# Kernel tuning notes

Measured on AMD Instinct MI355X. Metric: run time of the kernel, lower is better.

Reference implementation:

```python
import jax, jax.numpy as jnp
import numpy as np
from jax import lax

T = 16384          # num_tokens
H = 512            # hidden_size
HC = 4             # hc_mult
NGRAM = 4          # max_ngram_size -> conv dilation
N_EMBED = 256      # n_embed_per_ngram
N_HEADPN = 4       # n_head_per_ngram
NUM_HEADS = (NGRAM - 1) * N_HEADPN          # 12 embedding heads
HEAD_DIM = N_EMBED // N_HEADPN              # 64
E = (NGRAM - 1) * N_EMBED                   # 768 = engram_hidden_size
VOCAB = 50000
K = 4              # conv kernel_size
EPS = 1e-5         # layernorm_eps
GATE_EPS = 1e-6


def setup_inputs() -> dict:
    key = jax.random.key(0)
    ks = jax.random.split(key, 8)
    hash_ids = jax.random.randint(ks[0], (T, NUM_HEADS), 0, VOCAB, dtype=jnp.int32)
    offsets = jnp.asarray(np.concatenate([[0], np.cumsum([VOCAB] * (NUM_HEADS - 1))]).astype(np.int32))
    embedding_weight = jax.random.normal(ks[1], (NUM_HEADS * VOCAB, HEAD_DIM), jnp.float32) * 0.02
    key_projs_w = jax.random.normal(ks[2], (HC, E, H), jnp.float32) * 0.02
    q_norm_w = jnp.ones((HC, H), jnp.float32)
    k_norm_w = jnp.ones((HC, H), jnp.float32)
    v_proj_w = jax.random.normal(ks[3], (E, H), jnp.float32) * 0.02
    conv_w = jax.random.normal(ks[4], (HC * H, K), jnp.float32) * 0.1
    conv_norm_w = jnp.ones((HC, H), jnp.float32)
    hidden_states = jax.random.normal(ks[5], (T, HC, H), jnp.float32)
    return {
        'hash_ids': hash_ids, 'offsets': offsets, 'embedding_weight': embedding_weight,
        'key_projs_w': key_projs_w, 'q_norm_w': q_norm_w, 'k_norm_w': k_norm_w,
        'v_proj_w': v_proj_w, 'conv_w': conv_w, 'conv_norm_w': conv_norm_w,
        'hidden_states': hidden_states,
    }


def _group_rms_norm(x, w, eps=EPS):
    # x: [G, T, H], w: [G, H]; RMS over last dim, per-group affine scale
    inv = lax.rsqrt(jnp.mean(x * x, axis=-1, keepdims=True) + eps)
    return x * inv * w[:, None, :]


def reference(hash_ids, offsets, embedding_weight, key_projs_w, q_norm_w, k_norm_w,
              v_proj_w, conv_w, conv_norm_w, hidden_states):
    num_tokens, hc_mult, hidden = hidden_states.shape
    # --- MultiHeadEmbedding: hash-indexed gather into a concatenated table ---
    emb = embedding_weight[hash_ids + offsets[None, :]]          # [T, NUM_HEADS, HEAD_DIM]
    emb = emb.reshape(num_tokens, E)                              # [T, E]
    # --- key projection per hc group (bmm) ---
    keys = jnp.einsum('te,geh->gth', emb, key_projs_w)            # [HC, T, H]
    key_n = _group_rms_norm(keys, k_norm_w)
    query_n = _group_rms_norm(hidden_states.transpose(1, 0, 2), q_norm_w)  # [HC, T, H]
    # --- scaled dot-product gate ---
    scale = 1.0 / jnp.sqrt(jnp.asarray(hidden, hidden_states.dtype))
    gate = jax.nn.sigmoid(jnp.sum(key_n * query_n, axis=-1) * scale)       # [HC, T]
    gate = gate.T[:, :, None]                                     # [T, HC, 1]
    # --- value projection + gating ---
    value = gate * (emb @ v_proj_w)[:, None, :]                   # [T, HC, H]
    # --- ShortConv: GroupRMSNorm + depthwise dilated causal conv1d + SiLU ---
    x_n = _group_rms_norm(value.transpose(1, 0, 2), conv_norm_w)  # [HC, T, H]
    x_bct = x_n.transpose(0, 2, 1).reshape(1, hc_mult * hidden, num_tokens)  # [1, C, T]
    pad = NGRAM * (K - 1)
    y = lax.conv_general_dilated(
        x_bct, conv_w[:, None, :],                                # kernel [C, 1, K]
        window_strides=(1,), padding=[(pad, 0)], rhs_dilation=(NGRAM,),
        feature_group_count=hc_mult * hidden,
        dimension_numbers=('NCH', 'OIH', 'NCH'))
    y = jax.nn.silu(y)[0]                                         # [C, T]
    y = y.reshape(hc_mult, hidden, num_tokens).transpose(2, 0, 1) # [T, HC, H]
    return value + y


if __name__ == '__main__':
    out = reference(**setup_inputs())
    print(out.shape, out.dtype)
```

## Files before the change

kernel.cpp:

```cpp
#include <hip/hip_runtime.h>
#include <hip/hip_bf16.h>
#include <math.h>

#define T_TOK  16384
#define H_DIM  512
#define NHEADS 12
#define E_DIM  768
#define EPS_N  1e-5f
#define QK_SCALE 0.04419417382415922f

typedef unsigned short u16;
typedef __bf16 bf16;
typedef bf16   bf16x8 __attribute__((ext_vector_type(8)));
typedef float  f32x4  __attribute__((ext_vector_type(4)));
typedef u16    u16x8  __attribute__((ext_vector_type(8)));

__device__ __forceinline__ u16 f2bf(float f) {
  unsigned u = __builtin_bit_cast(unsigned, f);
  unsigned r = u + 0x7fffu + ((u >> 16) & 1u);
  return (u16)(r >> 16);
}
__device__ __forceinline__ float bf2f(u16 h) {
  unsigned u = ((unsigned)h) << 16;
  return __builtin_bit_cast(float, u);
}

__global__ __launch_bounds__(256) void gather_emb(
    const int* __restrict__ hash_ids, const int* __restrict__ offsets,
    const float* __restrict__ emb_w, u16* __restrict__ emb) {
  int idx = blockIdx.x * 256 + threadIdx.x;
  int pair = idx >> 3;
  int sub = idx & 7;
  int t = pair / 12;
  int head = pair - t * 12;
  int row = hash_ids[pair] + offsets[head];
  const float* src = emb_w + (size_t)row * 64 + sub * 8;
  float4 a = *(const float4*)src;
  float4 b = *(const float4*)(src + 4);
  u16x8 o;
  o[0] = f2bf(a.x); o[1] = f2bf(a.y); o[2] = f2bf(a.z); o[3] = f2bf(a.w);
  o[4] = f2bf(b.x); o[5] = f2bf(b.y); o[6] = f2bf(b.z); o[7] = f2bf(b.w);
  *(u16x8*)(emb + (size_t)t * E_DIM + head * 64 + sub * 8) = o;
}

__global__ __launch_bounds__(256) void build_wcat(
    const float* __restrict__ kp, const float* __restrict__ vp,
    u16* __restrict__ wt) {
  __shared__ float tile[32][33];
  int m = blockIdx.z;
  const float* src = (m < 4) ? (kp + (size_t)m * E_DIM * H_DIM) : vp;
  int h0 = blockIdx.x * 32, e0 = blockIdx.y * 32;
  int tx = threadIdx.x, ty = threadIdx.y;
  #pragma unroll
  for (int j = 0; j < 32; j += 8)
    tile[ty + j][tx] = src[(size_t)(e0 + ty + j) * H_DIM + h0 + tx];
  __syncthreads();
  #pragma unroll
  for (int j = 0; j < 32; j += 8) {
    int h = h0 + ty + j, e = e0 + tx;
    wt[(size_t)(m * H_DIM + h) * E_DIM + e] = f2bf(tile[tx][ty + j]);
  }
}

__global__ __launch_bounds__(256) void build_wc(
    const float* __restrict__ conv_w, const float* __restrict__ cnw,
    float* __restrict__ wc) {
  int cf = blockIdx.x * 256 + threadIdx.x;
  float c = cnw[cf];
  #pragma unroll
  for (int k = 0; k < 4; ++k) wc[k * 2048 + cf] = conv_w[cf * 4 + k] * c;
}

__global__ __launch_bounds__(256, 2) void gemm_bf16(
    const u16* __restrict__ A, const u16* __restrict__ BT,
    const float* __restrict__ hidden, const float* __restrict__ qw,
    const float* __restrict__ kw,
    u16* __restrict__ V, float* __restrict__ kssP, float* __restrict__ qkP,
    float* __restrict__ qssP, float* __restrict__ msvP) {
  __shared__ u16 As[128][64];
  __shared__ u16 Bs[128][64];
  __shared__ float part[2][128][3];
  const int K = E_DIM;
  int tid = threadIdx.x;
  int lane = tid & 63, wid = tid >> 6;
  int bx = blockIdx.x, by = blockIdx.y;
  int wm = (wid >> 1) * 64, wn = (wid & 1) * 64;
  int widN = wid & 1;

  const u16* aptr = A + (size_t)(by * 128 + (tid >> 3)) * K + (tid & 7) * 8;
  const u16* bptr = BT + (size_t)(bx * 128 + (tid >> 3)) * K + (tid & 7) * 8;
  int lds_off = tid * 16;

  f32x4 acc[4][4] = {};

  for (int k0 = 0; k0 < K; k0 += 64) {
    #pragma unroll
    for (int r = 0; r < 4; ++r) {
      __builtin_amdgcn_global_load_lds(
        (const __attribute__((address_space(1))) void*)(aptr + (size_t)(r * 32) * K + k0),
        (__attribute__((address_space(3))) void*)((char*)&As[0][0] + r * 4096 + lds_off),
        16, 0, 0);
      __builtin_amdgcn_global_load_lds(
        (const __attribute__((address_space(1))) void*)(bptr + (size_t)(r * 32) * K + k0),
        (__attribute__((address_space(3))) void*)((char*)&Bs[0][0] + r * 4096 + lds_off),
        16, 0, 0);
    }
    __syncthreads();
    int lr = lane & 15, lk8 = (lane >> 4) * 8;
    #pragma unroll
    for (int kk = 0; kk < 2; ++kk) {
      bf16x8 af[4], bfv[4];
      #pragma unroll
      for (int m = 0; m < 4; ++m)
        af[m] = *reinterpret_cast<const bf16x8*>(&As[wm + m * 16 + lr][kk * 32 + lk8]);
      #pragma unroll
      for (int n = 0; n < 4; ++n)
        bfv[n] = *reinterpret_cast<const bf16x8*>(&Bs[wn + n * 16 + lr][kk * 32 + lk8]);
      #pragma unroll
      for (int m = 0; m < 4; ++m)
        #pragma unroll
        for (int n = 0; n < 4; ++n)
          acc[m][n] = __builtin_amdgcn_mfma_f32_16x16x32_bf16(af[m], bfv[n], acc[m][n], 0, 0, 0);
    }
    __syncthreads();
  }

  int lr16 = lane & 15, rgrp = lane >> 4;

  if (bx < 16) {
    int g = bx >> 2, q = bx & 3;
    int colbase = g * 512 + q * 128 + wn + lr16;
    float qwv[4], kwv[4];
    #pragma unroll
    for (int n = 0; n < 4; ++n) {
      qwv[n] = qw[colbase + n * 16];
      kwv[n] = kw[colbase + n * 16];
    }
    #pragma unroll
    for (int m = 0; m < 4; ++m) {
      #pragma unroll
      for (int j = 0; j < 4; ++j) {
        int r = wm + m * 16 + rgrp * 4 + j;
        size_t t = (size_t)(by * 128 + r);
        float sk2 = 0.f, sqk = 0.f, sq2 = 0.f;
        #pragma unroll
        for (int n = 0; n < 4; ++n) {
          float kv = acc[m][n][j];
          float qv = hidden[t * 2048 + colbase + n * 16];
          sk2 += kv * kv;
          sqk += (qv * qwv[n]) * (kv * kwv[n]);
          sq2 += qv * qv;
        }
        #pragma unroll
        for (int off = 1; off < 16; off <<= 1) {
          sk2 += __shfl_xor(sk2, off, 64);
          sqk += __shfl_xor(sqk, off, 64);
          sq2 += __shfl_xor(sq2, off, 64);
        }
        if (lr16 == 0) {
          part[widN][r][0] = sk2;
          part[widN][r][1] = sqk;
          part[widN][r][2] = sq2;
        }
      }
    }
    __syncthreads();
    if (tid < 128) {
      int t = by * 128 + tid;
      int o = (t * 4 + g) * 4 + q;
      kssP[o] = part[0][tid][0] + part[1][tid][0];
      qkP[o]  = part[0][tid][1] + part[1][tid][1];
      qssP[o] = part[0][tid][2] + part[1][tid][2];
    }
  } else {
    int q2 = bx - 16;
    #pragma unroll
    for (int m = 0; m < 4; ++m) {
      #pragma unroll
      for (int j = 0; j < 4; ++j) {
        int r = wm + m * 16 + rgrp * 4 + j;
        size_t t = (size_t)(by * 128 + r);
        float sv2 = 0.f;
        #pragma unroll
        for (int n = 0; n < 4; ++n) {
          float v = acc[m][n][j];
          sv2 += v * v;
          V[t * 512 + q2 * 128 + wn + n * 16 + lr16] = f2bf(v);
        }
        #pragma unroll
        for (int off = 1; off < 16; off <<= 1) sv2 += __shfl_xor(sv2, off, 64);
        if (lr16 == 0) part[widN][r][0] = sv2;
      }
    }
    __syncthreads();
    if (tid < 128) {
      int t = by * 128 + tid;
      msvP[t * 4 + q2] = part[0][tid][0] + part[1][tid][0];
    }
  }
}

__global__ __launch_bounds__(256) void gate_finish(
    const float* __restrict__ kssP, const float* __restrict__ qkP,
    const float* __restrict__ qssP, const float* __restrict__ msvP,
    float* __restrict__ gateA, float* __restrict__ aA) {
  int i = blockIdx.x * 256 + threadIdx.x;
  int t = i >> 2;
  float4 k4 = *(const float4*)&kssP[i * 4];
  float4 d4 = *(const float4*)&qkP[i * 4];
  float4 q4 = *(const float4*)&qssP[i * 4];
  float4 m4 = *(const float4*)&msvP[t * 4];
  float kss = k4.x + k4.y + k4.z + k4.w;
  float qk  = d4.x + d4.y + d4.z + d4.w;
  float qss = q4.x + q4.y + q4.z + q4.w;
  float msv = (m4.x + m4.y + m4.z + m4.w) * (1.0f / 512.0f);
  float qinv = rsqrtf(qss * (1.0f / 512.0f) + EPS_N);
  float kinv = rsqrtf(kss * (1.0f / 512.0f) + EPS_N);
  float gate = 1.0f / (1.0f + __expf(-qk * qinv * kinv * QK_SCALE));
  gateA[i] = gate;
  aA[i] = gate * rsqrtf(gate * gate * msv + EPS_N);
}

__global__ __launch_bounds__(256) void out_kernel(
    const u16* __restrict__ V,
    const float* __restrict__ gateA, const float* __restrict__ aA,
    const float* __restrict__ wc,
    float* __restrict__ out) {
  int idx = blockIdx.x * 256 + threadIdx.x;
  int t = idx >> 8;
  int c8 = (idx & 255) * 8;
  int g = c8 >> 9;
  int h = c8 & 511;

  float acc[8] = {0.f, 0.f, 0.f, 0.f, 0.f, 0.f, 0.f, 0.f};
  float vr_t[8];
  #pragma unroll
  for (int k = 0; k < 4; ++k) {
    int tk = t - 12 + 4 * k;
    if (tk < 0) continue;
    float s = aA[tk * 4 + g];
    u16x8 vv = *(const u16x8*)&V[(size_t)tk * 512 + h];
    float4 w0 = *(const float4*)(wc + k * 2048 + c8);
    float4 w1 = *(const float4*)(wc + k * 2048 + c8 + 4);
    float w8[8] = {w0.x, w0.y, w0.z, w0.w, w1.x, w1.y, w1.z, w1.w};
    #pragma unroll
    for (int j = 0; j < 8; ++j) {
      float v = bf2f(vv[j]);
      acc[j] += w8[j] * s * v;
      if (k == 3) vr_t[j] = v;
    }
  }
  float gate = gateA[t * 4 + g];
  float r[8];
  #pragma unroll
  for (int j = 0; j < 8; ++j) {
    float y = acc[j];
    r[j] = gate * vr_t[j] + y / (1.0f + __expf(-y));
  }
  float* op = out + (size_t)t * 2048 + c8;
  *(float4*)op       = make_float4(r[0], r[1], r[2], r[3]);
  *(float4*)(op + 4) = make_float4(r[4], r[5], r[6], r[7]);
}

extern "C" void kernel_launch(void* const* d_in, const int* in_sizes, int n_in,
                              void* d_out, int out_size, void* d_ws, size_t ws_size,
                              hipStream_t stream) {
  const int*   hash_ids = (const int*)d_in[0];
  const int*   offsets  = (const int*)d_in[1];
  const float* emb_w    = (const float*)d_in[2];
  const float* kp       = (const float*)d_in[3];
  const float* qw       = (const float*)d_in[4];
  const float* kw       = (const float*)d_in[5];
  const float* vp       = (const float*)d_in[6];
  const float* conv_w   = (const float*)d_in[7];
  const float* cw       = (const float*)d_in[8];
  const float* hidden   = (const float*)d_in[9];
  float* out = (float*)d_out;
  char*  ws  = (char*)d_ws;

  u16*   V     = (u16*)ws;
  u16*   emb   = (u16*)(ws + 16777216);
  u16*   wt    = (u16*)(ws + 41943040);
  float* kssP  = (float*)(ws + 45875200);
  float* qkP   = (float*)(ws + 46923776);
  float* qssP  = (float*)(ws + 47972352);
  float* msvP  = (float*)(ws + 49020928);
  float* gateA = (float*)(ws + 49283072);
  float* aA    = (float*)(ws + 49545216);
  float* wc    = (float*)(ws + 49807360);

  gather_emb<<<(T_TOK * 12 * 8) / 256, 256, 0, stream>>>(hash_ids, offsets, emb_w, emb);
  build_wcat<<<dim3(16, 24, 5), dim3(32, 8), 0, stream>>>(kp, vp, wt);
  build_wc<<<8, 256, 0, stream>>>(conv_w, cw, wc);
  gemm_bf16<<<dim3(20, 128), 256, 0, stream>>>(emb, wt, hidden, qw, kw,
                                               V, kssP, qkP, qssP, msvP);
  gate_finish<<<(T_TOK * 4) / 256, 256, 0, stream>>>(kssP, qkP, qssP, msvP, gateA, aA);
  out_kernel<<<T_TOK * 256 / 256, 256, 0, stream>>>(V, gateA, aA, wc, out);
}
```

Before: 196.6 us.

## Precompute weighted bf16 query in fragment layout and per-token query norms

Adds a prep_q kernel that reads hidden_states once, computes the per-group query sum of squares, and writes q*q_norm_w as bf16 in a layout matching the GEMM accumulator fragments. The GEMM epilogue then reads packed bf16 query vectors, prefetched before the K loop, instead of strided fp32 hidden loads, and no longer computes the query norm. This aims to cut scattered fp32 reads in the epilogue and overlap the query fetch with the main loop. The cost is an extra kernel launch, an extra full pass over hidden plus a 64 MB intermediate write and read, higher register pressure from holding qf across the GEMM, and bf16 rounding of the query.

```diff
diff --git a/kernel.cpp b/kernel.cpp
--- a/kernel.cpp
+++ b/kernel.cpp
@@ -13,6 +13,7 @@
 typedef __bf16 bf16;
 typedef bf16   bf16x8 __attribute__((ext_vector_type(8)));
 typedef float  f32x4  __attribute__((ext_vector_type(4)));
+typedef u16    u16x4  __attribute__((ext_vector_type(4)));
 typedef u16    u16x8  __attribute__((ext_vector_type(8)));
 
 __device__ __forceinline__ u16 f2bf(float f) {
@@ -23,6 +24,11 @@
 __device__ __forceinline__ float bf2f(u16 h) {
   unsigned u = ((unsigned)h) << 16;
   return __builtin_bit_cast(float, u);
+}
+__device__ __forceinline__ float wave_sum(float v) {
+  #pragma unroll
+  for (int off = 32; off; off >>= 1) v += __shfl_xor(v, off, 64);
+  return v;
 }
 
 __global__ __launch_bounds__(256) void gather_emb(
@@ -71,25 +77,67 @@
   for (int k = 0; k < 4; ++k) wc[k * 2048 + cf] = conv_w[cf * 4 + k] * c;
 }
 
+__global__ __launch_bounds__(256) void prep_q(
+    const float* __restrict__ hidden, const float* __restrict__ qw,
+    u16* __restrict__ qhp, float* __restrict__ qssA) {
+  int t = blockIdx.x;
+  int g = threadIdx.x >> 6;
+  int lane = threadIdx.x & 63;
+  int sg = lane >> 4, lr = lane & 15;
+  float q2 = 0.f;
+  #pragma unroll
+  for (int bb = 0; bb < 2; ++bb) {
+    int b = g * 8 + sg + bb * 4;
+    const float* hp = hidden + (size_t)t * 2048 + b * 64 + lr;
+    u16x4 o;
+    #pragma unroll
+    for (int n = 0; n < 4; ++n) {
+      float q = hp[n * 16];
+      float w = qw[b * 64 + n * 16 + lr];
+      q2 += q * q;
+      o[n] = f2bf(q * w);
+    }
+    *(u16x4*)(qhp + (size_t)t * 2048 + b * 64 + lr * 4) = o;
+  }
+  q2 = wave_sum(q2);
+  if (lane == 0) qssA[t * 4 + g] = q2;
+}
+
 __global__ __launch_bounds__(256, 2) void gemm_bf16(
     const u16* __restrict__ A, const u16* __restrict__ BT,
-    const float* __restrict__ hidden, const float* __restrict__ qw,
-    const float* __restrict__ kw,
+    const u16* __restrict__ qhp, const float* __restrict__ kw,
     u16* __restrict__ V, float* __restrict__ kssP, float* __restrict__ qkP,
-    float* __restrict__ qssP, float* __restrict__ msvP) {
+    float* __restrict__ msvP) {
   __shared__ u16 As[128][64];
   __shared__ u16 Bs[128][64];
-  __shared__ float part[2][128][3];
+  __shared__ float part[2][128][2];
   const int K = E_DIM;
   int tid = threadIdx.x;
   int lane = tid & 63, wid = tid >> 6;
   int bx = blockIdx.x, by = blockIdx.y;
   int wm = (wid >> 1) * 64, wn = (wid & 1) * 64;
   int widN = wid & 1;
+  int lr16 = lane & 15, rgrp = lane >> 4;
 
   const u16* aptr = A + (size_t)(by * 128 + (tid >> 3)) * K + (tid & 7) * 8;
   const u16* bptr = BT + (size_t)(bx * 128 + (tid >> 3)) * K + (tid & 7) * 8;
   int lds_off = tid * 16;
+
+  u16x4 qf[4][4];
+  float kwv[4];
+  if (bx < 16) {
+    int g = bx >> 2, qq = bx & 3;
+    int cb = (g * 8 + qq * 2 + (wn >> 6)) * 64 + lr16 * 4;
+    #pragma unroll
+    for (int m = 0; m < 4; ++m)
+      #pragma unroll
+      for (int j = 0; j < 4; ++j)
+        qf[m][j] = *(const u16x4*)(qhp +
+            (size_t)(by * 128 + wm + m * 16 + rgrp * 4 + j) * 2048 + cb);
+    int colbase = g * 512 + qq * 128 + wn + lr16;
+    #pragma unroll
+    for (int n = 0; n < 4; ++n) kwv[n] = kw[colbase + n * 16];
+  }
 
   f32x4 acc[4][4] = {};
 
@@ -106,16 +154,16 @@
         16, 0, 0);
     }
     __syncthreads();
-    int lr = lane & 15, lk8 = (lane >> 4) * 8;
+    int lk8 = (lane >> 4) * 8;
     #pragma unroll
     for (int kk = 0; kk < 2; ++kk) {
       bf16x8 af[4], bfv[4];
       #pragma unroll
       for (int m = 0; m < 4; ++m)
-        af[m] = *reinterpret_cast<const bf16x8*>(&As[wm + m * 16 + lr][kk * 32 + lk8]);
+        af[m] = *reinterpret_cast<const bf16x8*>(&As[wm + m * 16 + lr16][kk * 32 + lk8]);
       #pragma unroll
       for (int n = 0; n < 4; ++n)
-        bfv[n] = *reinterpret_cast<const bf16x8*>(&Bs[wn + n * 16 + lr][kk * 32 + lk8]);
+        bfv[n] = *reinterpret_cast<const bf16x8*>(&Bs[wn + n * 16 + lr16][kk * 32 + lk8]);
       #pragma unroll
       for (int m = 0; m < 4; ++m)
         #pragma unroll
@@ -125,55 +173,41 @@
     __syncthreads();
   }
 
-  int lr16 = lane & 15, rgrp = lane >> 4;
-
   if (bx < 16) {
-    int g = bx >> 2, q = bx & 3;
-    int colbase = g * 512 + q * 128 + wn + lr16;
-    float qwv[4], kwv[4];
-    #pragma unroll
-    for (int n = 0; n < 4; ++n) {
-      qwv[n] = qw[colbase + n * 16];
-      kwv[n] = kw[colbase + n * 16];
-    }
+    int g = bx >> 2, qq = bx & 3;
     #pragma unroll
     for (int m = 0; m < 4; ++m) {
       #pragma unroll
       for (int j = 0; j < 4; ++j) {
         int r = wm + m * 16 + rgrp * 4 + j;
-        size_t t = (size_t)(by * 128 + r);
-        float sk2 = 0.f, sqk = 0.f, sq2 = 0.f;
+        float sk2 = 0.f, sqk = 0.f;
         #pragma unroll
         for (int n = 0; n < 4; ++n) {
           float kv = acc[m][n][j];
-          float qv = hidden[t * 2048 + colbase + n * 16];
+          float qv = bf2f(qf[m][j][n]);
           sk2 += kv * kv;
-          sqk += (qv * qwv[n]) * (kv * kwv[n]);
-          sq2 += qv * qv;
+          sqk += qv * (kv * kwv[n]);
         }
         #pragma unroll
         for (int off = 1; off < 16; off <<= 1) {
           sk2 += __shfl_xor(sk2, off, 64);
           sqk += __shfl_xor(sqk, off, 64);
-          sq2 += __shfl_xor(sq2, off, 64);
         }
         if (lr16 == 0) {
           part[widN][r][0] = sk2;
           part[widN][r][1] = sqk;
-          part[widN][r][2] = sq2;
         }
       }
     }
     __syncthreads();
     if (tid < 128) {
       int t = by * 128 + tid;
-      int o = (t * 4 + g) * 4 + q;
+      int o = (t * 4 + g) * 4 + qq;
       kssP[o] = part[0][tid][0] + part[1][tid][0];
       qkP[o]  = part[0][tid][1] + part[1][tid][1];
-      qssP[o] = part[0][tid][2] + part[1][tid][2];
     }
   } else {
-    int q2 = bx - 16;
+    int q2i = bx - 16;
     #pragma unroll
     for (int m = 0; m < 4; ++m) {
       #pragma unroll
@@ -185,7 +219,7 @@
         for (int n = 0; n < 4; ++n) {
           float v = acc[m][n][j];
           sv2 += v * v;
-          V[t * 512 + q2 * 128 + wn + n * 16 + lr16] = f2bf(v);
+          V[t * 512 + q2i * 128 + wn + n * 16 + lr16] = f2bf(v);
         }
         #pragma unroll
         for (int off = 1; off < 16; off <<= 1) sv2 += __shfl_xor(sv2, off, 64);
@@ -195,24 +229,23 @@
     __syncthreads();
     if (tid < 128) {
       int t = by * 128 + tid;
-      msvP[t * 4 + q2] = part[0][tid][0] + part[1][tid][0];
+      msvP[t * 4 + q2i] = part[0][tid][0] + part[1][tid][0];
     }
   }
 }
 
 __global__ __launch_bounds__(256) void gate_finish(
     const float* __restrict__ kssP, const float* __restrict__ qkP,
-    const float* __restrict__ qssP, const float* __restrict__ msvP,
+    const float* __restrict__ qssA, const float* __restrict__ msvP,
     float* __restrict__ gateA, float* __restrict__ aA) {
   int i = blockIdx.x * 256 + threadIdx.x;
   int t = i >> 2;
   float4 k4 = *(const float4*)&kssP[i * 4];
   float4 d4 = *(const float4*)&qkP[i * 4];
-  float4 q4 = *(const float4*)&qssP[i * 4];
   float4 m4 = *(const float4*)&msvP[t * 4];
   float kss = k4.x + k4.y + k4.z + k4.w;
   float qk  = d4.x + d4.y + d4.z + d4.w;
-  float qss = q4.x + q4.y + q4.z + q4.w;
+  float qss = qssA[i];
   float msv = (m4.x + m4.y + m4.z + m4.w) * (1.0f / 512.0f);
   float qinv = rsqrtf(qss * (1.0f / 512.0f) + EPS_N);
   float kinv = rsqrtf(kss * (1.0f / 512.0f) + EPS_N);
@@ -281,19 +314,21 @@
   u16*   V     = (u16*)ws;
   u16*   emb   = (u16*)(ws + 16777216);
   u16*   wt    = (u16*)(ws + 41943040);
-  float* kssP  = (float*)(ws + 45875200);
-  float* qkP   = (float*)(ws + 46923776);
-  float* qssP  = (float*)(ws + 47972352);
-  float* msvP  = (float*)(ws + 49020928);
-  float* gateA = (float*)(ws + 49283072);
-  float* aA    = (float*)(ws + 49545216);
-  float* wc    = (float*)(ws + 49807360);
+  u16*   qhp   = (u16*)(ws + 45875200);
+  float* kssP  = (float*)(ws + 112984064);
+  float* qkP   = (float*)(ws + 114032640);
+  float* qssA  = (float*)(ws + 115081216);
+  float* msvP  = (float*)(ws + 115343360);
+  float* gateA = (float*)(ws + 115605504);
+  float* aA    = (float*)(ws + 115867648);
+  float* wc    = (float*)(ws + 116129792);
 
   gather_emb<<<(T_TOK * 12 * 8) / 256, 256, 0, stream>>>(hash_ids, offsets, emb_w, emb);
   build_wcat<<<dim3(16, 24, 5), dim3(32, 8), 0, stream>>>(kp, vp, wt);
   build_wc<<<8, 256, 0, stream>>>(conv_w, cw, wc);
-  gemm_bf16<<<dim3(20, 128), 256, 0, stream>>>(emb, wt, hidden, qw, kw,
-                                               V, kssP, qkP, qssP, msvP);
-  gate_finish<<<(T_TOK * 4) / 256, 256, 0, stream>>>(kssP, qkP, qssP, msvP, gateA, aA);
+  prep_q<<<T_TOK, 256, 0, stream>>>(hidden, qw, qhp, qssA);
+  gemm_bf16<<<dim3(20, 128), 256, 0, stream>>>(emb, wt, qhp, kw,
+                                               V, kssP, qkP, msvP);
+  gate_finish<<<(T_TOK * 4) / 256, 256, 0, stream>>>(kssP, qkP, qssA, msvP, gateA, aA);
   out_kernel<<<T_TOK * 256 / 256, 256, 0, stream>>>(V, gateA, aA, wc, out);
 }
```

Result: slower. 215.1 us (+9.4%).
